# Kernel optimization log

Hardware: AMD Instinct MI355X
Metric: run time of the kernel (lower is better)

Reference implementation:

```python
import jax, jax.numpy as jnp
import numpy as np

B, S1, S2, D, H, FFN = 4, 1024, 1024, 1024, 16, 4096
DK = D // H  # 64
EPS = 1e-5


def layer_norm(x, g, b):
    m = jnp.mean(x, axis=-1, keepdims=True)
    v = jnp.mean((x - m) ** 2, axis=-1, keepdims=True)
    return (x - m) * jax.lax.rsqrt(v + EPS) * g + b


def cross_attention(y, kvn, mask, qw, kw, vw, ow, ob):
    # y: [B,S1,D], kvn: [B,S2,D], mask: [B,S2] int (0 -> masked)
    q = (y @ qw).reshape(B, S1, H, DK)
    k = (kvn @ kw).reshape(B, S2, H, DK)
    v = (kvn @ vw).reshape(B, S2, H, DK)
    attn = jnp.einsum('bqhd,bkhd->bhqk', q, k) / np.sqrt(DK).astype(np.float32)
    attn = jnp.where(mask[:, None, None, :] == 0, jnp.float32(-1e9), attn)
    attn = jax.nn.softmax(attn, axis=-1)
    out = jnp.einsum('bhqk,bkhd->bqhd', attn, v).reshape(B, S1, H * DK)
    return out @ ow + ob


def setup_inputs() -> dict:
    key = jax.random.key(0)
    ks = jax.random.split(key, 16)
    s = 1.0 / np.sqrt(D)
    inp = {
        'x': jax.random.normal(ks[0], (B, S1, D), jnp.float32),
        'kv': jax.random.normal(ks[1], (B, S2, D), jnp.float32),
        'attn_bias': jax.random.randint(ks[2], (B, S2), 0, 2, jnp.int32),
        'ln1_g': jnp.ones((D,), jnp.float32),
        'ln1_b': jnp.zeros((D,), jnp.float32),
        'qw0': jax.random.normal(ks[3], (D, D), jnp.float32) * s,
        'kw0': jax.random.normal(ks[4], (D, D), jnp.float32) * s,
        'vw0': jax.random.normal(ks[5], (D, D), jnp.float32) * s,
        'ow0': jax.random.normal(ks[6], (D, D), jnp.float32) * s,
        'ob0': jnp.zeros((D,), jnp.float32),
        'qw1': jax.random.normal(ks[7], (D, D), jnp.float32) * s,
        'kw1': jax.random.normal(ks[8], (D, D), jnp.float32) * s,
        'vw1': jax.random.normal(ks[9], (D, D), jnp.float32) * s,
        'ow1': jax.random.normal(ks[10], (D, D), jnp.float32) * s,
        'ob1': jnp.zeros((D,), jnp.float32),
        'ln2_g': jnp.ones((D,), jnp.float32),
        'ln2_b': jnp.zeros((D,), jnp.float32),
        'w1': jax.random.normal(ks[11], (D, FFN), jnp.float32) * s,
        'b1': jnp.zeros((FFN,), jnp.float32),
        'w2': jax.random.normal(ks[12], (FFN, D), jnp.float32) * (1.0 / np.sqrt(FFN)),
        'b2': jnp.zeros((D,), jnp.float32),
    }
    return inp


def reference(x, kv, attn_bias, ln1_g, ln1_b, qw0, kw0, vw0, ow0, ob0,
              qw1, kw1, vw1, ow1, ob1, ln2_g, ln2_b, w1, b1, w2, b2):
    y = layer_norm(x, ln1_g, ln1_b)
    kvn = layer_norm(kv, ln1_g, ln1_b)  # same norm module applied to both
    y = cross_attention(y, kvn, attn_bias, qw0, kw0, vw0, ow0, ob0) + y
    y = cross_attention(y, kvn, attn_bias, qw1, kw1, vw1, ow1, ob1) + y
    x = x + y  # dropout rate 0 -> identity
    y = layer_norm(x, ln2_g, ln2_b)
    y = jax.nn.relu(y @ w1 + b1) @ w2 + b2
    x = x + y
    return x
```

## Files before the change

kernel.cpp:

```cpp
#include <hip/hip_runtime.h>
#include <stdint.h>

typedef unsigned short u16;
typedef __bf16 bf16x8 __attribute__((ext_vector_type(8)));
typedef float f32x4 __attribute__((ext_vector_type(4)));

#define LOG2E 1.4426950408889634f

__device__ __forceinline__ float bf2f(u16 a) {
  union { unsigned u; float f; } v; v.u = ((unsigned)a) << 16; return v.f;
}
__device__ __forceinline__ u16 f2bf(float f) {
  union { float f; unsigned u; } v; v.f = f;
  unsigned r = v.u + 0x7fffu + ((v.u >> 16) & 1u);
  return (u16)(r >> 16);
}
__device__ __forceinline__ u16 f2bf_fast(float f) {
  __bf16 h = (__bf16)f;
  union { __bf16 h; u16 u; } v; v.h = h; return v.u;
}
__device__ __forceinline__ void gl_lds16(const void* g, void* l) {
  __builtin_amdgcn_global_load_lds(
      (const __attribute__((address_space(1))) uint32_t*)g,
      (__attribute__((address_space(3))) uint32_t*)l,
      16, 0, 0);
}

__device__ __forceinline__ int swz(int row, int colu16) {
  return row * 64 + (colu16 ^ (((row ^ (row >> 2)) & 7) << 3));
}

template <int BM, int BN, int MODE>
__global__ __launch_bounds__(256) void gemm_bt(
    const u16* __restrict__ A, const u16* __restrict__ Bt,
    u16* Cbf, float* C32,
    const float* __restrict__ bias,
    const u16* resbf, const float* __restrict__ resx,
    int M, int N, int K)
{
  constexpr int MT = BM / 32, NT = BN / 32;
  constexpr int GA = BM / 32, GB = BN / 32;
  __shared__ u16 sA[BM * 64];
  __shared__ u16 sB[BN * 64];
  const int tid  = threadIdx.x;
  const int wave = tid >> 6, lane = tid & 63;
  const int quad = lane >> 4, l16 = lane & 15;
  const int wm = wave >> 1, wn = wave & 1;
  const int m0 = blockIdx.y * BM, n0 = blockIdx.x * BN;

  f32x4 acc[MT][NT] = {};

  for (int k0 = 0; k0 < K; k0 += 64) {
    __syncthreads();
#pragma unroll
    for (int i = 0; i < GA; ++i) {
      int cb = i * 256 + wave * 64;
      int c = cb + lane;
      int row = c >> 3, kc = c & 7;
      gl_lds16(A + (size_t)(m0 + row) * K + k0 + kc * 8, &sA[cb * 8]);
    }
#pragma unroll
    for (int i = 0; i < GB; ++i) {
      int cb = i * 256 + wave * 64;
      int c = cb + lane;
      int row = c >> 3, kc = c & 7;
      gl_lds16(Bt + (size_t)(n0 + row) * K + k0 + kc * 8, &sB[cb * 8]);
    }
    __syncthreads();

#pragma unroll
    for (int kk = 0; kk < 2; ++kk) {
      bf16x8 fa[MT], fb[NT];
#pragma unroll
      for (int mt = 0; mt < MT; ++mt)
        fa[mt] = *(const bf16x8*)&sA[(wm * (BM / 2) + mt * 16 + l16) * 64 + kk * 32 + quad * 8];
#pragma unroll
      for (int nt = 0; nt < NT; ++nt)
        fb[nt] = *(const bf16x8*)&sB[(wn * (BN / 2) + nt * 16 + l16) * 64 + kk * 32 + quad * 8];
#pragma unroll
      for (int mt = 0; mt < MT; ++mt)
#pragma unroll
        for (int nt = 0; nt < NT; ++nt)
          acc[mt][nt] = __builtin_amdgcn_mfma_f32_16x16x32_bf16(
              fa[mt], fb[nt], acc[mt][nt], 0, 0, 0);
    }
  }

#pragma unroll
  for (int mt = 0; mt < MT; ++mt) {
#pragma unroll
    for (int nt = 0; nt < NT; ++nt) {
#pragma unroll
      for (int r = 0; r < 4; ++r) {
        int row = m0 + wm * (BM / 2) + mt * 16 + quad * 4 + r;
        int col = n0 + wn * (BN / 2) + nt * 16 + l16;
        size_t idx = (size_t)row * N + col;
        float v = acc[mt][nt][r];
        if constexpr (MODE == 0) {
          Cbf[idx] = f2bf(v);
        } else if constexpr (MODE == 1) {
          v += bias[col] + bf2f(resbf[idx]);
          Cbf[idx] = f2bf(v);
        } else if constexpr (MODE == 2) {
          v = fmaxf(v + bias[col], 0.f);
          Cbf[idx] = f2bf(v);
        } else if constexpr (MODE == 3) {
          v += bias[col] + resx[idx] + bf2f(resbf[idx]);
          C32[idx] = v;
        } else {
          C32[idx] = C32[idx] + v;
        }
      }
    }
  }
}

__global__ __launch_bounds__(256) void transpose64(
    const float* __restrict__ in, u16* __restrict__ out, int R, int Cstride)
{
  __shared__ u16 tile[64][72];
  const int r0 = blockIdx.y * 64, c0 = blockIdx.x * 64;
  const int t = threadIdx.x;
  {
    const int lr = t >> 4, lc = (t & 15) * 4;
#pragma unroll
    for (int h = 0; h < 4; ++h) {
      int row = h * 16 + lr;
      float4 vd = *(const float4*)&in[(size_t)(r0 + row) * Cstride + c0 + lc];
      ushort4 ov;
      ov.x = f2bf(vd.x); ov.y = f2bf(vd.y); ov.z = f2bf(vd.z); ov.w = f2bf(vd.w);
      *(ushort4*)&tile[row][lc] = ov;
    }
  }
  __syncthreads();
  {
    const int lr = t >> 3, lv = t & 7;
#pragma unroll
    for (int h = 0; h < 2; ++h) {
      int orow = h * 32 + lr;
      u16 tmp[8];
#pragma unroll
      for (int j = 0; j < 8; ++j) tmp[j] = tile[lv * 8 + j][orow];
      *(uint4*)&out[(size_t)(c0 + orow) * R + r0 + lv * 8] = *(uint4*)tmp;
    }
  }
}

__global__ __launch_bounds__(256) void vt_kernel(
    const u16* __restrict__ in, u16* __restrict__ out)
{
  __shared__ u16 tile[64][72];
  const int st = blockIdx.x, bh = blockIdx.y;
  const int b = bh >> 4, h = bh & 15;
  const int t = threadIdx.x;
  const int lr = t >> 3, lv = t & 7;
  const u16* src = in + ((size_t)b * 1024 + st * 64) * 2048 + 1024 + h * 64;
#pragma unroll
  for (int half = 0; half < 2; ++half) {
    int row = half * 32 + lr;
    uint4 vd = *(const uint4*)&src[(size_t)row * 2048 + lv * 8];
    *(uint4*)&tile[row][lv * 8] = vd;
  }
  __syncthreads();
  u16* dst = out + (size_t)bh * 64 * 1024 + st * 64;
#pragma unroll
  for (int half = 0; half < 2; ++half) {
    int orow = half * 32 + lr;
    u16 tmp[8];
#pragma unroll
    for (int j = 0; j < 8; ++j) tmp[j] = tile[lv * 8 + j][orow];
    *(uint4*)&dst[(size_t)orow * 1024 + lv * 8] = *(uint4*)tmp;
  }
}

__global__ __launch_bounds__(256) void ln_kernel(
    const float* __restrict__ x, const float* __restrict__ g,
    const float* __restrict__ b, u16* __restrict__ outbf)
{
  const int row = blockIdx.x, t = threadIdx.x;
  const int wave = t >> 6, lane = t & 63;
  float4 xv = *(const float4*)&x[(size_t)row * 1024 + t * 4];
  float v0 = xv.x, v1 = xv.y, v2 = xv.z, v3 = xv.w;
  float s = v0 + v1 + v2 + v3;
  float s2 = v0 * v0 + v1 * v1 + v2 * v2 + v3 * v3;
  for (int m = 1; m < 64; m <<= 1) { s += __shfl_xor(s, m); s2 += __shfl_xor(s2, m); }
  __shared__ float ps[4], pq[4];
  if (lane == 0) { ps[wave] = s; pq[wave] = s2; }
  __syncthreads();
  s = ps[0] + ps[1] + ps[2] + ps[3];
  s2 = pq[0] + pq[1] + pq[2] + pq[3];
  float mean = s * (1.f / 1024.f);
  float var = s2 * (1.f / 1024.f) - mean * mean;
  float rs = rsqrtf(var + 1e-5f);
  float4 gv = *(const float4*)&g[t * 4];
  float4 bv = *(const float4*)&b[t * 4];
  ushort4 ov;
  ov.x = f2bf((v0 - mean) * rs * gv.x + bv.x);
  ov.y = f2bf((v1 - mean) * rs * gv.y + bv.y);
  ov.z = f2bf((v2 - mean) * rs * gv.z + bv.z);
  ov.w = f2bf((v3 - mean) * rs * gv.w + bv.w);
  *(ushort4*)&outbf[(size_t)row * 1024 + t * 4] = ov;
}

__global__ __launch_bounds__(256) void ln_add_kernel(
    const float* __restrict__ x, const u16* __restrict__ ybf,
    const float* __restrict__ g, const float* __restrict__ b,
    u16* __restrict__ hbf)
{
  const int row = blockIdx.x, t = threadIdx.x;
  const int wave = t >> 6, lane = t & 63;
  float4 xv = *(const float4*)&x[(size_t)row * 1024 + t * 4];
  ushort4 yv = *(const ushort4*)&ybf[(size_t)row * 1024 + t * 4];
  float v0 = xv.x + bf2f(yv.x), v1 = xv.y + bf2f(yv.y);
  float v2 = xv.z + bf2f(yv.z), v3 = xv.w + bf2f(yv.w);
  float s = v0 + v1 + v2 + v3;
  float s2 = v0 * v0 + v1 * v1 + v2 * v2 + v3 * v3;
  for (int m = 1; m < 64; m <<= 1) { s += __shfl_xor(s, m); s2 += __shfl_xor(s2, m); }
  __shared__ float ps[4], pq[4];
  if (lane == 0) { ps[wave] = s; pq[wave] = s2; }
  __syncthreads();
  s = ps[0] + ps[1] + ps[2] + ps[3];
  s2 = pq[0] + pq[1] + pq[2] + pq[3];
  float mean = s * (1.f / 1024.f);
  float var = s2 * (1.f / 1024.f) - mean * mean;
  float rs = rsqrtf(var + 1e-5f);
  float4 gv = *(const float4*)&g[t * 4];
  float4 bv = *(const float4*)&b[t * 4];
  ushort4 ov;
  ov.x = f2bf((v0 - mean) * rs * gv.x + bv.x);
  ov.y = f2bf((v1 - mean) * rs * gv.y + bv.y);
  ov.z = f2bf((v2 - mean) * rs * gv.z + bv.z);
  ov.w = f2bf((v3 - mean) * rs * gv.w + bv.w);
  *(ushort4*)&hbf[(size_t)row * 1024 + t * 4] = ov;
}

__global__ __launch_bounds__(256) void attn_kernel(
    const u16* __restrict__ Q,
    const u16* __restrict__ K,
    const u16* __restrict__ Vt,
    const int* __restrict__ mask,
    u16* __restrict__ O)
{
  __shared__ u16 sK[64 * 64], sVt[64 * 64], sP[128 * 64];
  __shared__ float smaskf[64];
  const int h = blockIdx.x, qt = blockIdx.y, b = blockIdx.z;
  const int t = threadIdx.x;
  const int wave = t >> 6, lane = t & 63;
  const int quad = lane >> 4, l16 = lane & 15;
  const u16* Qb = Q + (size_t)b * 1024 * 1024 + (size_t)qt * 128 * 1024 + h * 64;
  const u16* Kb = K + (size_t)b * 1024 * 2048 + h * 64;
  const u16* Vb = Vt + (size_t)(b * 16 + h) * 64 * 1024;

#pragma unroll
  for (int i = 0; i < 4; ++i) {
    int cb = i * 256 + wave * 64;
    int c = cb + lane;
    int row = c >> 3;
    int scc = (c & 7) ^ ((row ^ (row >> 2)) & 7);
    gl_lds16(Qb + (size_t)row * 1024 + scc * 8, &sP[cb * 8]);
  }
  __syncthreads();
  bf16x8 aq[2][2];
#pragma unroll
  for (int g = 0; g < 2; ++g)
#pragma unroll
    for (int ks = 0; ks < 2; ++ks)
      aq[g][ks] = *(const bf16x8*)&sP[swz(wave * 32 + g * 16 + l16, ks * 32 + quad * 8)];

  float m2_[2][4], l_[2][4];
  f32x4 accO[2][4] = {};
#pragma unroll
  for (int g = 0; g < 2; ++g)
#pragma unroll
    for (int r = 0; r < 4; ++r) { m2_[g][r] = -1e30f; l_[g][r] = 0.f; }

  constexpr float QS = 0.125f * LOG2E;

  for (int j = 0; j < 16; ++j) {
    __syncthreads();
#pragma unroll
    for (int i = 0; i < 2; ++i) {
      int cb = i * 256 + wave * 64;
      int c = cb + lane;
      int row = c >> 3;
      int scc = (c & 7) ^ ((row ^ (row >> 2)) & 7);
      gl_lds16(Kb + (size_t)(j * 64 + row) * 2048 + scc * 8, &sK[cb * 8]);
      gl_lds16(Vb + (size_t)row * 1024 + j * 64 + scc * 8, &sVt[cb * 8]);
    }
    if (t < 64) smaskf[t] = (mask[b * 1024 + j * 64 + t] == 0) ? -1e9f : 0.f;
    __syncthreads();

    float mf[4];
#pragma unroll
    for (int nt = 0; nt < 4; ++nt) mf[nt] = smaskf[nt * 16 + l16];

#pragma unroll
    for (int g = 0; g < 2; ++g) {
      f32x4 accS[4] = {};
#pragma unroll
      for (int ks = 0; ks < 2; ++ks) {
#pragma unroll
        for (int nt = 0; nt < 4; ++nt) {
          bf16x8 bk = *(const bf16x8*)&sK[swz(nt * 16 + l16, ks * 32 + quad * 8)];
          accS[nt] = __builtin_amdgcn_mfma_f32_16x16x32_bf16(aq[g][ks], bk, accS[nt], 0, 0, 0);
        }
      }
      float vv[4][4], cm_[4];
      bool need = false;
#pragma unroll
      for (int r = 0; r < 4; ++r) {
#pragma unroll
        for (int nt = 0; nt < 4; ++nt) vv[r][nt] = fmaf(accS[nt][r], QS, mf[nt]);
        float cm = fmaxf(fmaxf(vv[r][0], vv[r][1]), fmaxf(vv[r][2], vv[r][3]));
        for (int sh = 1; sh < 16; sh <<= 1) cm = fmaxf(cm, __shfl_xor(cm, sh));
        cm_[r] = cm;
        need = need || (cm > m2_[g][r] + 8.f);
      }
      if (__any(need)) {
#pragma unroll
        for (int r = 0; r < 4; ++r) {
          float nm = fmaxf(m2_[g][r], cm_[r]);
          float al = exp2f(m2_[g][r] - nm);
          m2_[g][r] = nm;
          l_[g][r] *= al;
#pragma unroll
          for (int n2 = 0; n2 < 4; ++n2) accO[g][n2][r] *= al;
        }
      }
#pragma unroll
      for (int r = 0; r < 4; ++r) {
        int prow = wave * 32 + g * 16 + quad * 4 + r;
        float rs = 0.f;
#pragma unroll
        for (int nt = 0; nt < 4; ++nt) {
          float p = exp2f(vv[r][nt] - m2_[g][r]);
          rs += p;
          sP[swz(prow, nt * 16 + l16)] = f2bf_fast(p);
        }
        l_[g][r] += rs;
      }
    }
#pragma unroll
    for (int ks = 0; ks < 2; ++ks) {
      bf16x8 bv[4];
#pragma unroll
      for (int n2 = 0; n2 < 4; ++n2)
        bv[n2] = *(const bf16x8*)&sVt[swz(n2 * 16 + l16, ks * 32 + quad * 8)];
#pragma unroll
      for (int g = 0; g < 2; ++g) {
        bf16x8 ap = *(const bf16x8*)&sP[swz(wave * 32 + g * 16 + l16, ks * 32 + quad * 8)];
#pragma unroll
        for (int n2 = 0; n2 < 4; ++n2)
          accO[g][n2] = __builtin_amdgcn_mfma_f32_16x16x32_bf16(ap, bv[n2], accO[g][n2], 0, 0, 0);
      }
    }
  }

  u16* Ob = O + (size_t)b * 1024 * 1024 + (size_t)qt * 128 * 1024 + h * 64;
#pragma unroll
  for (int g = 0; g < 2; ++g) {
#pragma unroll
    for (int r = 0; r < 4; ++r) {
      float lr = l_[g][r];
      for (int sh = 1; sh < 16; sh <<= 1) lr += __shfl_xor(lr, sh);
      float inv = 1.f / lr;
      int row = wave * 32 + g * 16 + quad * 4 + r;
#pragma unroll
      for (int n2 = 0; n2 < 4; ++n2)
        Ob[(size_t)row * 1024 + n2 * 16 + l16] = f2bf_fast(accO[g][n2][r] * inv);
    }
  }
}

extern "C" void kernel_launch(void* const* d_in, const int* in_sizes, int n_in,
                              void* d_out, int out_size, void* d_ws, size_t ws_size,
                              hipStream_t stream)
{
  const float* x   = (const float*)d_in[0];
  const float* kv  = (const float*)d_in[1];
  const int* attn_bias = (const int*)d_in[2];
  const float* ln1_g = (const float*)d_in[3];
  const float* ln1_b = (const float*)d_in[4];
  const float* qw0 = (const float*)d_in[5];
  const float* kw0 = (const float*)d_in[6];
  const float* vw0 = (const float*)d_in[7];
  const float* ow0 = (const float*)d_in[8];
  const float* ob0 = (const float*)d_in[9];
  const float* qw1 = (const float*)d_in[10];
  const float* kw1 = (const float*)d_in[11];
  const float* vw1 = (const float*)d_in[12];
  const float* ow1 = (const float*)d_in[13];
  const float* ob1 = (const float*)d_in[14];
  const float* ln2_g = (const float*)d_in[15];
  const float* ln2_b = (const float*)d_in[16];
  const float* w1 = (const float*)d_in[17];
  const float* b1 = (const float*)d_in[18];
  const float* w2 = (const float*)d_in[19];
  const float* b2 = (const float*)d_in[20];

  char* ws = (char*)d_ws;
  const size_t MB = 1u << 20;
  u16* Wkv   = (u16*)(ws + 0 * MB);
  u16* Wsm   = (u16*)(ws + 4 * MB);
  u16* wtA   = (u16*)(ws + 0 * MB);
  u16* wtB   = (u16*)(ws + 4 * MB);
  u16* ybf   = (u16*)(ws + 8 * MB);
  u16* kvnbf = (u16*)(ws + 16 * MB);
  u16* qbuf  = (u16*)(ws + 24 * MB);
  u16* kvbuf = (u16*)(ws + 32 * MB);
  u16* hbf   = kvnbf;
  u16* fbuf  = kvbuf;
  u16* attnb = (u16*)d_out;
  u16* vT    = (u16*)((char*)d_out + 8 * MB);
  float* out32 = (float*)d_out;

  const dim3 B256(256);
  const dim3 gT(16, 16);
  const dim3 gGemmN1k(8, 64);
  const dim3 gGemm2k(16, 32);
  const dim3 gVt(16, 64);
  const dim3 gAttn(16, 8, 4);

  ln_kernel<<<4096, B256, 0, stream>>>(x,  ln1_g, ln1_b, ybf);
  ln_kernel<<<4096, B256, 0, stream>>>(kv, ln1_g, ln1_b, kvnbf);

  for (int layer = 0; layer < 2; ++layer) {
    const float* qw = layer ? qw1 : qw0;
    const float* kw = layer ? kw1 : kw0;
    const float* vw = layer ? vw1 : vw0;
    const float* ow = layer ? ow1 : ow0;
    const float* ob = layer ? ob1 : ob0;

    transpose64<<<gT, B256, 0, stream>>>(kw, Wkv, 1024, 1024);
    transpose64<<<gT, B256, 0, stream>>>(vw, Wkv + 1024 * 1024, 1024, 1024);
    gemm_bt<128, 128, 0><<<gGemm2k, B256, 0, stream>>>(
        kvnbf, Wkv, kvbuf, nullptr, nullptr, nullptr, nullptr, 4096, 2048, 1024);
    transpose64<<<gT, B256, 0, stream>>>(qw, Wsm, 1024, 1024);
    gemm_bt<64, 128, 0><<<gGemmN1k, B256, 0, stream>>>(
        ybf, Wsm, qbuf, nullptr, nullptr, nullptr, nullptr, 4096, 1024, 1024);
    vt_kernel<<<gVt, B256, 0, stream>>>(kvbuf, vT);

    attn_kernel<<<gAttn, B256, 0, stream>>>(qbuf, kvbuf, vT, attn_bias, attnb);

    transpose64<<<gT, B256, 0, stream>>>(ow, Wsm, 1024, 1024);
    gemm_bt<64, 128, 1><<<gGemmN1k, B256, 0, stream>>>(
        attnb, Wsm, ybf, nullptr, ob, ybf, nullptr, 4096, 1024, 1024);
  }

  ln_add_kernel<<<4096, B256, 0, stream>>>(x, ybf, ln2_g, ln2_b, hbf);

  for (int band = 0; band < 2; ++band) {
    transpose64<<<dim3(32, 16), B256, 0, stream>>>(w1 + band * 2048, wtA, 1024, 4096);
    transpose64<<<dim3(16, 32), B256, 0, stream>>>(w2 + (size_t)band * 2048 * 1024,
                                                   wtB, 2048, 1024);
    gemm_bt<128, 128, 2><<<gGemm2k, B256, 0, stream>>>(
        hbf, wtA, fbuf, nullptr, b1 + band * 2048, nullptr, nullptr,
        4096, 2048, 1024);
    if (band == 0) {
      gemm_bt<64, 128, 3><<<gGemmN1k, B256, 0, stream>>>(
          fbuf, wtB, nullptr, out32, b2, ybf, x, 4096, 1024, 2048);
    } else {
      gemm_bt<64, 128, 4><<<gGemmN1k, B256, 0, stream>>>(
          fbuf, wtB, nullptr, out32, nullptr, nullptr, nullptr, 4096, 1024, 2048);
    }
  }
}
```

Baseline: 616.7 us.

## Compact unmasked keys and skip masked KV tiles in attention; shrink GEMM tiles

A new scan kernel builds, per batch, a compacted list of unmasked key positions and their count. The V-transpose kernel and the attention kernel gather K and V rows through that list, and the attention loop only covers the tiles holding valid keys, with padding inside the last tile masked by position. This removes the QK and PV work, and the loads, for keys that would get softmax weight of effectively zero. Separately, the 2048-wide GEMMs switch from 128-row to 64-row tiles with twice the grid. That gives more workgroups, at the cost of less reuse of each loaded tile. A batch with every key masked would give n=0 and an index of -1, which differs from the reference's uniform softmax.

```diff
diff --git a/kernel.cpp b/kernel.cpp
--- a/kernel.cpp
+++ b/kernel.cpp
@@ -146,20 +146,48 @@
   }
 }
 
-__global__ __launch_bounds__(256) void vt_kernel(
-    const u16* __restrict__ in, u16* __restrict__ out)
+__global__ __launch_bounds__(256) void mask_scan(
+    const int* __restrict__ mask, int* __restrict__ sidx, int* __restrict__ nv)
+{
+  const int b = blockIdx.x, t = threadIdx.x;
+  const int wave = t >> 6, lane = t & 63;
+  int m[4]; int cnt = 0;
+#pragma unroll
+  for (int k = 0; k < 4; ++k) { m[k] = (mask[b * 1024 + t * 4 + k] != 0); cnt += m[k]; }
+  int sc = cnt;
+  for (int sh = 1; sh < 64; sh <<= 1) {
+    int u = __shfl_up(sc, sh);
+    if (lane >= sh) sc += u;
+  }
+  __shared__ int wsum[4];
+  if (lane == 63) wsum[wave] = sc;
+  __syncthreads();
+  int woff = 0;
+  for (int w = 0; w < wave; ++w) woff += wsum[w];
+  int pos = woff + sc - cnt;
+#pragma unroll
+  for (int k = 0; k < 4; ++k)
+    if (m[k]) sidx[b * 1024 + pos++] = t * 4 + k;
+  if (t == 255) nv[b] = wsum[0] + wsum[1] + wsum[2] + wsum[3];
+}
+
+__global__ __launch_bounds__(256) void vtc_kernel(
+    const u16* __restrict__ in, const int* __restrict__ sidx,
+    const int* __restrict__ nv, u16* __restrict__ out)
 {
   __shared__ u16 tile[64][72];
   const int st = blockIdx.x, bh = blockIdx.y;
   const int b = bh >> 4, h = bh & 15;
   const int t = threadIdx.x;
   const int lr = t >> 3, lv = t & 7;
-  const u16* src = in + ((size_t)b * 1024 + st * 64) * 2048 + 1024 + h * 64;
+  const int n = nv[b];
+  const u16* srcb = in + (size_t)b * 1024 * 2048 + 1024 + h * 64;
 #pragma unroll
   for (int half = 0; half < 2; ++half) {
-    int row = half * 32 + lr;
-    uint4 vd = *(const uint4*)&src[(size_t)row * 2048 + lv * 8];
-    *(uint4*)&tile[row][lv * 8] = vd;
+    int i = st * 64 + half * 32 + lr;
+    int s = sidx[b * 1024 + (i < n ? i : n - 1)];
+    uint4 vd = *(const uint4*)&srcb[(size_t)s * 2048 + lv * 8];
+    *(uint4*)&tile[half * 32 + lr][lv * 8] = vd;
   }
   __syncthreads();
   u16* dst = out + (size_t)bh * 64 * 1024 + st * 64;
@@ -238,11 +266,11 @@
     const u16* __restrict__ Q,
     const u16* __restrict__ K,
     const u16* __restrict__ Vt,
-    const int* __restrict__ mask,
+    const int* __restrict__ sidx,
+    const int* __restrict__ nvp,
     u16* __restrict__ O)
 {
   __shared__ u16 sK[64 * 64], sVt[64 * 64], sP[128 * 64];
-  __shared__ float smaskf[64];
   const int h = blockIdx.x, qt = blockIdx.y, b = blockIdx.z;
   const int t = threadIdx.x;
   const int wave = t >> 6, lane = t & 63;
@@ -250,6 +278,9 @@
   const u16* Qb = Q + (size_t)b * 1024 * 1024 + (size_t)qt * 128 * 1024 + h * 64;
   const u16* Kb = K + (size_t)b * 1024 * 2048 + h * 64;
   const u16* Vb = Vt + (size_t)(b * 16 + h) * 64 * 1024;
+  const int n = nvp[b];
+  const int jmax = (n + 63) >> 6;
+  const int* sb = sidx + b * 1024;
 
 #pragma unroll
   for (int i = 0; i < 4; ++i) {
@@ -276,7 +307,7 @@
 
   constexpr float QS = 0.125f * LOG2E;
 
-  for (int j = 0; j < 16; ++j) {
+  for (int j = 0; j < jmax; ++j) {
     __syncthreads();
 #pragma unroll
     for (int i = 0; i < 2; ++i) {
@@ -284,15 +315,17 @@
       int c = cb + lane;
       int row = c >> 3;
       int scc = (c & 7) ^ ((row ^ (row >> 2)) & 7);
-      gl_lds16(Kb + (size_t)(j * 64 + row) * 2048 + scc * 8, &sK[cb * 8]);
+      int gi = j * 64 + row;
+      int s = sb[gi < n ? gi : n - 1];
+      gl_lds16(Kb + (size_t)s * 2048 + scc * 8, &sK[cb * 8]);
       gl_lds16(Vb + (size_t)row * 1024 + j * 64 + scc * 8, &sVt[cb * 8]);
     }
-    if (t < 64) smaskf[t] = (mask[b * 1024 + j * 64 + t] == 0) ? -1e9f : 0.f;
     __syncthreads();
 
     float mf[4];
 #pragma unroll
-    for (int nt = 0; nt < 4; ++nt) mf[nt] = smaskf[nt * 16 + l16];
+    for (int nt = 0; nt < 4; ++nt)
+      mf[nt] = (j * 64 + nt * 16 + l16 < n) ? 0.f : -1e9f;
 
 #pragma unroll
     for (int g = 0; g < 2; ++g) {
@@ -402,6 +435,8 @@
   const size_t MB = 1u << 20;
   u16* Wkv   = (u16*)(ws + 0 * MB);
   u16* Wsm   = (u16*)(ws + 4 * MB);
+  int* sidx  = (int*)(ws + 6 * MB);
+  int* nvp   = sidx + 4096;
   u16* wtA   = (u16*)(ws + 0 * MB);
   u16* wtB   = (u16*)(ws + 4 * MB);
   u16* ybf   = (u16*)(ws + 8 * MB);
@@ -417,9 +452,11 @@
   const dim3 B256(256);
   const dim3 gT(16, 16);
   const dim3 gGemmN1k(8, 64);
-  const dim3 gGemm2k(16, 32);
+  const dim3 gGemm2k(16, 64);
   const dim3 gVt(16, 64);
   const dim3 gAttn(16, 8, 4);
+
+  mask_scan<<<4, B256, 0, stream>>>(attn_bias, sidx, nvp);
 
   ln_kernel<<<4096, B256, 0, stream>>>(x,  ln1_g, ln1_b, ybf);
   ln_kernel<<<4096, B256, 0, stream>>>(kv, ln1_g, ln1_b, kvnbf);
@@ -433,14 +470,14 @@
 
     transpose64<<<gT, B256, 0, stream>>>(kw, Wkv, 1024, 1024);
     transpose64<<<gT, B256, 0, stream>>>(vw, Wkv + 1024 * 1024, 1024, 1024);
-    gemm_bt<128, 128, 0><<<gGemm2k, B256, 0, stream>>>(
+    gemm_bt<64, 128, 0><<<gGemm2k, B256, 0, stream>>>(
         kvnbf, Wkv, kvbuf, nullptr, nullptr, nullptr, nullptr, 4096, 2048, 1024);
     transpose64<<<gT, B256, 0, stream>>>(qw, Wsm, 1024, 1024);
     gemm_bt<64, 128, 0><<<gGemmN1k, B256, 0, stream>>>(
         ybf, Wsm, qbuf, nullptr, nullptr, nullptr, nullptr, 4096, 1024, 1024);
-    vt_kernel<<<gVt, B256, 0, stream>>>(kvbuf, vT);
-
-    attn_kernel<<<gAttn, B256, 0, stream>>>(qbuf, kvbuf, vT, attn_bias, attnb);
+    vtc_kernel<<<gVt, B256, 0, stream>>>(kvbuf, sidx, nvp, vT);
+
+    attn_kernel<<<gAttn, B256, 0, stream>>>(qbuf, kvbuf, vT, sidx, nvp, attnb);
 
     transpose64<<<gT, B256, 0, stream>>>(ow, Wsm, 1024, 1024);
     gemm_bt<64, 128, 1><<<gGemmN1k, B256, 0, stream>>>(
@@ -453,7 +490,7 @@
     transpose64<<<dim3(32, 16), B256, 0, stream>>>(w1 + band * 2048, wtA, 1024, 4096);
     transpose64<<<dim3(16, 32), B256, 0, stream>>>(w2 + (size_t)band * 2048 * 1024,
                                                    wtB, 2048, 1024);
-    gemm_bt<128, 128, 2><<<gGemm2k, B256, 0, stream>>>(
+    gemm_bt<64, 128, 2><<<gGemm2k, B256, 0, stream>>>(
         hbf, wtA, fbuf, nullptr, b1 + band * 2048, nullptr, nullptr,
         4096, 2048, 1024);
     if (band == 0) {
```

After: 584.6 us. -5.2%, faster.
